# Optimization experiments

Measured on AMD Instinct MI355X. Metric: run time of the kernel, lower is better.

Reference implementation:

```python
import jax, jax.numpy as jnp
import numpy as np

L, B, S, D, H, FF = 6, 4, 1024, 256, 8, 128
DH = D // H
EPS = 1e-5


def _ln(x, w, b):
    m = x.mean(-1, keepdims=True)
    v = ((x - m) ** 2).mean(-1, keepdims=True)
    return (x - m) / jnp.sqrt(v + EPS) * w + b


def setup_inputs() -> dict:
    key = jax.random.key(0)
    ks = jax.random.split(key, 6)
    s = lambda k, shape: jax.random.normal(k, shape, jnp.float32) * 0.02
    return {
        "x": jax.random.normal(ks[0], (B, S, D), jnp.float32),
        "ln1_w": jnp.ones((L, D), jnp.float32),
        "ln1_b": jnp.zeros((L, D), jnp.float32),
        "wqkv": s(ks[1], (L, D, 3 * D)),   # qkv_linear, bias=False
        "wout": s(ks[2], (L, D, D)),       # out_linear, bias=False
        "ln2_w": jnp.ones((L, D), jnp.float32),
        "ln2_b": jnp.zeros((L, D), jnp.float32),
        "w1": s(ks[3], (L, D, 2 * FF)),    # Linear(d_model, 2*ff)
        "b1": jnp.zeros((L, 2 * FF), jnp.float32),
        "w2": s(ks[4], (L, FF, D)),        # Linear(ff, d_model)
        "b2": jnp.zeros((L, D), jnp.float32),
    }


def reference(x, ln1_w, ln1_b, wqkv, wout, ln2_w, ln2_b, w1, b1, w2, b2):
    attn_weights_list = []
    scale = 1.0 / jnp.sqrt(jnp.float32(DH))
    for i in range(L):
        # --- pre-norm multi-head attention ---
        xn = _ln(x, ln1_w[i], ln1_b[i])
        qkv = xn @ wqkv[i]                       # [B,S,3D]
        q, k, v = jnp.split(qkv, 3, axis=-1)
        rs = lambda t: t.reshape(B, S, H, DH).transpose(0, 2, 1, 3)  # b h s d
        q, k, v = rs(q), rs(k), rs(v)
        logits = jnp.einsum('bhid,bhjd->bhij', q, k) * scale
        aw = jax.nn.softmax(logits, axis=-1)     # [B,H,S,S] (dropout=0, eval)
        attn_weights_list.append(aw)
        o = jnp.einsum('bhij,bhjd->bhid', aw, v)
        o = o.transpose(0, 2, 1, 3).reshape(B, S, D) @ wout[i]
        x = x + o
        # --- pre-norm GEGLU FFN ---
        h = _ln(x, ln2_w[i], ln2_b[i]) @ w1[i] + b1[i]   # [B,S,2*FF]
        a, g = jnp.split(h, 2, axis=-1)
        x = x + (a * jax.nn.gelu(g, approximate=False)) @ w2[i] + b2[i]
    return x, jnp.stack(attn_weights_list)      # [B,S,D], [L,B,H,S,S]
```

## Files before the change

kernel.cpp:

```cpp
#include <hip/hip_runtime.h>
#include <hip/hip_bf16.h>

typedef __bf16 bf16x8 __attribute__((ext_vector_type(8)));
typedef __bf16 bf16x4 __attribute__((ext_vector_type(4)));
typedef __bf16 bf16x2 __attribute__((ext_vector_type(2)));
typedef float  f32x4  __attribute__((ext_vector_type(4)));

#define LAYERS 6
#define BATCH  4
#define SEQ    1024
#define DMODEL 256
#define NHEAD  8
#define DHEAD  32
#define FFDIM  128
#define ROWS   (BATCH*SEQ)
#define QKVN   (3*DMODEL)
#define QSCALE 0.2550348616f

static __device__ __forceinline__ bf16x8 ldg8(const __bf16* p) {
  return *reinterpret_cast<const bf16x8*>(p);
}
#define MFMA16(a, b, c) __builtin_amdgcn_mfma_f32_16x16x32_bf16((a), (b), (c), 0, 0, 0)

__global__ void k_prep(const float* __restrict__ wqkv, const float* __restrict__ wout,
                       const float* __restrict__ w1, const float* __restrict__ w2,
                       __bf16* __restrict__ wqkvT, __bf16* __restrict__ woutT,
                       __bf16* __restrict__ w1T, __bf16* __restrict__ w2T) {
  const int N1 = LAYERS * DMODEL * QKVN;
  const int N2 = LAYERS * DMODEL * DMODEL;
  const int N3 = LAYERS * DMODEL * 2 * FFDIM;
  const int N4 = LAYERS * FFDIM * DMODEL;
  int total = N1 + N2 + N3 + N4;
  for (int i = blockIdx.x * blockDim.x + threadIdx.x; i < total; i += gridDim.x * blockDim.x) {
    int j = i;
    if (j < N1) {
      int l = j / (DMODEL * QKVN), rc = j - l * (DMODEL * QKVN);
      int r = rc / QKVN, c = rc - r * QKVN;
      wqkvT[(size_t)l * DMODEL * QKVN + (size_t)c * DMODEL + r] = (__bf16)wqkv[j]; continue;
    } j -= N1;
    if (j < N2) {
      int l = j / (DMODEL * DMODEL), rc = j - l * (DMODEL * DMODEL);
      int r = rc / DMODEL, c = rc - r * DMODEL;
      woutT[(size_t)l * DMODEL * DMODEL + (size_t)c * DMODEL + r] = (__bf16)wout[j]; continue;
    } j -= N2;
    if (j < N3) {
      int l = j / (DMODEL * 2 * FFDIM), rc = j - l * (DMODEL * 2 * FFDIM);
      int r = rc / (2 * FFDIM), c = rc - r * (2 * FFDIM);
      w1T[(size_t)l * DMODEL * 2 * FFDIM + (size_t)c * DMODEL + r] = (__bf16)w1[j]; continue;
    } j -= N3;
    {
      int l = j / (FFDIM * DMODEL), rc = j - l * (FFDIM * DMODEL);
      int r = rc / DMODEL, c = rc - r * DMODEL;
      w2T[(size_t)l * FFDIM * DMODEL + (size_t)c * FFDIM + r] = (__bf16)w2[j];
    }
  }
}

__global__ __launch_bounds__(64) void k_ln(const float* __restrict__ x,
                                           const float* __restrict__ w,
                                           const float* __restrict__ b,
                                           __bf16* __restrict__ out) {
  int row = blockIdx.x, l = threadIdx.x;
  const float* xr = x + (size_t)row * DMODEL;
  float v[4];
  #pragma unroll
  for (int j = 0; j < 4; ++j) v[j] = xr[l + 64 * j];
  float s = v[0] + v[1] + v[2] + v[3];
  #pragma unroll
  for (int off = 32; off >= 1; off >>= 1) s += __shfl_xor(s, off);
  float mean = s * (1.0f / DMODEL);
  float sq = 0.f;
  #pragma unroll
  for (int j = 0; j < 4; ++j) { v[j] -= mean; sq += v[j] * v[j]; }
  #pragma unroll
  for (int off = 32; off >= 1; off >>= 1) sq += __shfl_xor(sq, off);
  float rstd = rsqrtf(sq * (1.0f / DMODEL) + 1e-5f);
  __bf16* orow = out + (size_t)row * DMODEL;
  #pragma unroll
  for (int j = 0; j < 4; ++j) {
    int c = l + 64 * j;
    orow[c] = (__bf16)(v[j] * rstd * w[c] + b[c]);
  }
}

__global__ __launch_bounds__(256) void k_qkv(const __bf16* __restrict__ xn,
                                             const __bf16* __restrict__ Bt,
                                             __bf16* __restrict__ qb,
                                             __bf16* __restrict__ kt,
                                             __bf16* __restrict__ vt) {
  int w = threadIdx.x >> 6, l = threadIdx.x & 63, lr = l & 15, lg = l >> 4;
  int m0 = blockIdx.x * 64 + w * 16;
  int n0 = blockIdx.y * 64;
  f32x4 acc[4] = {};
  const __bf16* ap = xn + (size_t)(m0 + lr) * DMODEL + 8 * lg;
  const __bf16* bp = Bt + (size_t)(n0 + lr) * DMODEL + 8 * lg;
  for (int kc = 0; kc < DMODEL; kc += 32) {
    bf16x8 a = ldg8(ap + kc);
    #pragma unroll
    for (int t = 0; t < 4; ++t) {
      bf16x8 b = ldg8(bp + (size_t)t * 16 * DMODEL + kc);
      acc[t] = MFMA16(a, b, acc[t]);
    }
  }
  int row = m0 + lg * 4;
  if (n0 < DMODEL) {
    #pragma unroll
    for (int t = 0; t < 4; ++t) {
      int col = n0 + t * 16 + lr;
      #pragma unroll
      for (int r = 0; r < 4; ++r)
        qb[(size_t)(row + r) * DMODEL + col] = (__bf16)(acc[t][r] * QSCALE);
    }
  } else if (n0 < 2 * DMODEL) {
    int b_ = row >> 10, s = row & (SEQ - 1);
    #pragma unroll
    for (int t = 0; t < 4; ++t) {
      int hdh = n0 - DMODEL + t * 16 + lr;
      int h = hdh >> 5, dh = hdh & 31;
      size_t base = ((size_t)(b_ * NHEAD + h) * SEQ + s) * DHEAD + dh;
      #pragma unroll
      for (int r = 0; r < 4; ++r) kt[base + (size_t)r * DHEAD] = (__bf16)acc[t][r];
    }
  } else {
    int b_ = row >> 10, s = row & (SEQ - 1);
    #pragma unroll
    for (int t = 0; t < 4; ++t) {
      int hdh = n0 - 2 * DMODEL + t * 16 + lr;
      int h = hdh >> 5, dh = hdh & 31;
      bf16x4 v4;
      #pragma unroll
      for (int r = 0; r < 4; ++r) v4[r] = (__bf16)acc[t][r];
      *reinterpret_cast<bf16x4*>(vt + ((size_t)(b_ * NHEAD + h) * DHEAD + dh) * SEQ + s) = v4;
    }
  }
}

__global__ __launch_bounds__(512, 4) void k_attn(const __bf16* __restrict__ qb,
                                                 const __bf16* __restrict__ kt,
                                                 const __bf16* __restrict__ vt,
                                                 __bf16* __restrict__ ob,
                                                 float* __restrict__ aw) {
  __shared__ __bf16 P[8][2][16][40];
  __shared__ float  Ssum[8][16];
  __shared__ float  OS[8][16][34];
  int bid = blockIdx.x;
  int swz = (bid & 7) * 256 + (bid >> 3);
  int qblk = swz & 63, h = (swz >> 6) & 7, b = swz >> 9;
  int w = threadIdx.x >> 6, l = threadIdx.x & 63, lr = l & 15, lg = l >> 4;
  int q0 = qblk * 16;
  bf16x8 qf = ldg8(qb + ((size_t)(b * SEQ) + q0 + lr) * DMODEL + h * DHEAD + 8 * lg);
  const __bf16* ktb = kt + (size_t)(b * NHEAD + h) * SEQ * DHEAD + 8 * lg;
  const __bf16* vtb = vt + (size_t)(b * NHEAD + h) * DHEAD * SEQ;
  f32x4 z = {};
  int kbeg = w * 128;

  f32x4 p[8];
  f32x4 accO[2] = {};

  #pragma unroll
  for (int j = 0; j < 4; ++j) {
    int kc = kbeg + j * 32;
    #pragma unroll
    for (int half = 0; half < 2; ++half) {
      int t = j * 2 + half;
      bf16x8 kf = ldg8(ktb + (size_t)(kc + half * 16 + lr) * DHEAD);
      f32x4 d = MFMA16(qf, kf, z);
      #pragma unroll
      for (int r = 0; r < 4; ++r) {
        p[t][r] = exp2f(d[r]);
        P[w][j & 1][lg * 4 + r][half * 16 + lr] = (__bf16)p[t][r];
      }
    }
    if (j > 0) {
      bf16x8 pf  = *reinterpret_cast<const bf16x8*>(&P[w][(j & 1) ^ 1][lr][8 * lg]);
      bf16x8 vf0 = ldg8(vtb + (size_t)lr * SEQ + (kc - 32) + 8 * lg);
      bf16x8 vf1 = ldg8(vtb + (size_t)(16 + lr) * SEQ + (kc - 32) + 8 * lg);
      accO[0] = MFMA16(pf, vf0, accO[0]);
      accO[1] = MFMA16(pf, vf1, accO[1]);
    }
  }
  {
    bf16x8 pf  = *reinterpret_cast<const bf16x8*>(&P[w][1][lr][8 * lg]);
    bf16x8 vf0 = ldg8(vtb + (size_t)lr * SEQ + (kbeg + 96) + 8 * lg);
    bf16x8 vf1 = ldg8(vtb + (size_t)(16 + lr) * SEQ + (kbeg + 96) + 8 * lg);
    accO[0] = MFMA16(pf, vf0, accO[0]);
    accO[1] = MFMA16(pf, vf1, accO[1]);
  }

  float s4[4] = {0.f, 0.f, 0.f, 0.f};
  #pragma unroll
  for (int t = 0; t < 8; ++t)
    #pragma unroll
    for (int r = 0; r < 4; ++r) s4[r] += p[t][r];
  #pragma unroll
  for (int off = 1; off < 16; off <<= 1) {
    #pragma unroll
    for (int r = 0; r < 4; ++r) s4[r] += __shfl_xor(s4[r], off);
  }
  if (lr == 0) {
    #pragma unroll
    for (int r = 0; r < 4; ++r) Ssum[w][lg * 4 + r] = s4[r];
  }
  __syncthreads();
  float rinv[4];
  #pragma unroll
  for (int r = 0; r < 4; ++r) {
    int row = lg * 4 + r;
    float s = Ssum[0][row] + Ssum[1][row] + Ssum[2][row] + Ssum[3][row]
            + Ssum[4][row] + Ssum[5][row] + Ssum[6][row] + Ssum[7][row];
    rinv[r] = 1.0f / s;
  }

  float* awb = aw + ((size_t)(b * NHEAD + h) * SEQ) * SEQ;
  #pragma unroll
  for (int t = 0; t < 8; ++t) {
    int k0 = kbeg + t * 16;
    #pragma unroll
    for (int r = 0; r < 4; ++r)
      __builtin_nontemporal_store(p[t][r] * rinv[r],
                                  &awb[(size_t)(q0 + lg * 4 + r) * SEQ + k0 + lr]);
  }

  #pragma unroll
  for (int t = 0; t < 2; ++t)
    #pragma unroll
    for (int r = 0; r < 4; ++r) OS[w][lg * 4 + r][t * 16 + lr] = accO[t][r] * rinv[r];
  __syncthreads();
  int row = threadIdx.x >> 5, col = threadIdx.x & 31;
  float o = 0.f;
  #pragma unroll
  for (int ww = 0; ww < 8; ++ww) o += OS[ww][row][col];
  ob[((size_t)(b * SEQ) + q0 + row) * DMODEL + h * DHEAD + col] = (__bf16)o;
}

template <int LAST>
__global__ __launch_bounds__(512) void k_pf(const __bf16* __restrict__ ob,
                                            const __bf16* __restrict__ woutT,
                                            const float* __restrict__ xres,
                                            const float* __restrict__ ln2w,
                                            const float* __restrict__ ln2b,
                                            const __bf16* __restrict__ w1t,
                                            const float* __restrict__ b1,
                                            const __bf16* __restrict__ w2t,
                                            const float* __restrict__ b2,
                                            float* __restrict__ x32out,
                                            const float* __restrict__ lnw_n,
                                            const float* __restrict__ lnb_n,
                                            const __bf16* __restrict__ wqkvT_n,
                                            __bf16* __restrict__ qb,
                                            __bf16* __restrict__ kt,
                                            __bf16* __restrict__ vt,
                                            float* __restrict__ xout) {
  __shared__ float  xs[16][268];
  __shared__ __bf16 XN[16][264];
  __shared__ __bf16 G[16][136];
  __shared__ __bf16 HT[16][136];
  int w = threadIdx.x >> 6, l = threadIdx.x & 63, lr = l & 15, lg = l >> 4;
  int m0 = blockIdx.x * 16;
  {
    int n0 = w * 32;
    f32x4 acc[2] = {};
    const __bf16* ap = ob + (size_t)(m0 + lr) * DMODEL + 8 * lg;
    const __bf16* bp = woutT + (size_t)(n0 + lr) * DMODEL + 8 * lg;
    for (int kc = 0; kc < DMODEL; kc += 32) {
      bf16x8 a = ldg8(ap + kc);
      #pragma unroll
      for (int t = 0; t < 2; ++t)
        acc[t] = MFMA16(a, ldg8(bp + (size_t)t * 16 * DMODEL + kc), acc[t]);
    }
    #pragma unroll
    for (int t = 0; t < 2; ++t) {
      int col = n0 + t * 16 + lr;
      #pragma unroll
      for (int r = 0; r < 4; ++r) {
        int row = lg * 4 + r;
        xs[row][col] = acc[t][r] + xres[(size_t)(m0 + row) * DMODEL + col];
      }
    }
  }
  __syncthreads();
  #pragma unroll
  for (int rr = 0; rr < 2; ++rr) {
    int row = w * 2 + rr;
    f32x4 v = *reinterpret_cast<const f32x4*>(&xs[row][4 * l]);
    float s = v[0] + v[1] + v[2] + v[3];
    #pragma unroll
    for (int off = 32; off >= 1; off >>= 1) s += __shfl_xor(s, off);
    float mean = s * (1.0f / DMODEL);
    float sq = 0.f;
    f32x4 c;
    #pragma unroll
    for (int j = 0; j < 4; ++j) { c[j] = v[j] - mean; sq += c[j] * c[j]; }
    #pragma unroll
    for (int off = 32; off >= 1; off >>= 1) sq += __shfl_xor(sq, off);
    float rstd = rsqrtf(sq * (1.0f / DMODEL) + 1e-5f);
    f32x4 lwv = *reinterpret_cast<const f32x4*>(&ln2w[4 * l]);
    f32x4 lbv = *reinterpret_cast<const f32x4*>(&ln2b[4 * l]);
    bf16x4 o4;
    #pragma unroll
    for (int j = 0; j < 4; ++j) o4[j] = (__bf16)(c[j] * rstd * lwv[j] + lbv[j]);
    *reinterpret_cast<bf16x4*>(&XN[row][4 * l]) = o4;
  }
  __syncthreads();
  int n0f = w * 32;
  f32x4 acc1[2] = {};
  {
    const __bf16* bp = w1t + (size_t)(n0f + lr) * DMODEL + 8 * lg;
    for (int kc = 0; kc < DMODEL; kc += 32) {
      bf16x8 a = *reinterpret_cast<const bf16x8*>(&XN[lr][kc + 8 * lg]);
      #pragma unroll
      for (int t = 0; t < 2; ++t)
        acc1[t] = MFMA16(a, ldg8(bp + (size_t)t * 16 * DMODEL + kc), acc1[t]);
    }
  }
  if (w >= 4) {
    #pragma unroll
    for (int t = 0; t < 2; ++t) {
      int col = n0f + t * 16 + lr;
      #pragma unroll
      for (int r = 0; r < 4; ++r) {
        float g = acc1[t][r] + b1[col];
        float ge = 0.5f * g * (1.0f + erff(g * 0.70710678118654752f));
        G[lg * 4 + r][col - 128] = (__bf16)ge;
      }
    }
  }
  __syncthreads();
  if (w < 4) {
    #pragma unroll
    for (int t = 0; t < 2; ++t) {
      int col = n0f + t * 16 + lr;
      #pragma unroll
      for (int r = 0; r < 4; ++r) {
        float a1 = acc1[t][r] + b1[col];
        HT[lg * 4 + r][col] = (__bf16)(a1 * (float)G[lg * 4 + r][col]);
      }
    }
  }
  __syncthreads();
  {
    f32x4 acc2[2] = {};
    const __bf16* bp = w2t + (size_t)(n0f + lr) * FFDIM + 8 * lg;
    for (int kc = 0; kc < FFDIM; kc += 32) {
      bf16x8 a2 = *reinterpret_cast<const bf16x8*>(&HT[lr][kc + 8 * lg]);
      #pragma unroll
      for (int t = 0; t < 2; ++t)
        acc2[t] = MFMA16(a2, ldg8(bp + (size_t)t * 16 * FFDIM + kc), acc2[t]);
    }
    #pragma unroll
    for (int t = 0; t < 2; ++t) {
      int col = n0f + t * 16 + lr;
      #pragma unroll
      for (int r = 0; r < 4; ++r) {
        int row = lg * 4 + r;
        xs[row][col] = acc2[t][r] + b2[col] + xs[row][col];
      }
    }
  }
  __syncthreads();
  #pragma unroll
  for (int rr = 0; rr < 2; ++rr) {
    int row = w * 2 + rr;
    f32x4 v = *reinterpret_cast<const f32x4*>(&xs[row][4 * l]);
    if (LAST) {
      *reinterpret_cast<f32x4*>(&xout[(size_t)(m0 + row) * DMODEL + 4 * l]) = v;
    } else {
      float s = v[0] + v[1] + v[2] + v[3];
      #pragma unroll
      for (int off = 32; off >= 1; off >>= 1) s += __shfl_xor(s, off);
      float mean = s * (1.0f / DMODEL);
      float sq = 0.f;
      f32x4 c;
      #pragma unroll
      for (int j = 0; j < 4; ++j) { c[j] = v[j] - mean; sq += c[j] * c[j]; }
      #pragma unroll
      for (int off = 32; off >= 1; off >>= 1) sq += __shfl_xor(sq, off);
      float rstd = rsqrtf(sq * (1.0f / DMODEL) + 1e-5f);
      *reinterpret_cast<f32x4*>(&x32out[(size_t)(m0 + row) * DMODEL + 4 * l]) = v;
      f32x4 lwv = *reinterpret_cast<const f32x4*>(&lnw_n[4 * l]);
      f32x4 lbv = *reinterpret_cast<const f32x4*>(&lnb_n[4 * l]);
      bf16x4 o4;
      #pragma unroll
      for (int j = 0; j < 4; ++j) o4[j] = (__bf16)(c[j] * rstd * lwv[j] + lbv[j]);
      *reinterpret_cast<bf16x4*>(&XN[row][4 * l]) = o4;
    }
  }
  if (!LAST) {
    __syncthreads();
    f32x4 acc[6] = {};
    {
      const __bf16* bp = wqkvT_n + (size_t)(w * 96 + lr) * DMODEL + 8 * lg;
      for (int kc = 0; kc < DMODEL; kc += 32) {
        bf16x8 a = *reinterpret_cast<const bf16x8*>(&XN[lr][kc + 8 * lg]);
        #pragma unroll
        for (int t = 0; t < 6; ++t)
          acc[t] = MFMA16(a, ldg8(bp + (size_t)t * 16 * DMODEL + kc), acc[t]);
      }
    }
    int row = m0 + lg * 4;
    int b_ = row >> 10, s = row & (SEQ - 1);
    #pragma unroll
    for (int t = 0; t < 6; ++t) {
      int col = w * 96 + t * 16 + lr;
      if (col < DMODEL) {
        #pragma unroll
        for (int r = 0; r < 4; ++r)
          qb[(size_t)(row + r) * DMODEL + col] = (__bf16)(acc[t][r] * QSCALE);
      } else if (col < 2 * DMODEL) {
        int hdh = col - DMODEL;
        int h = hdh >> 5, dh = hdh & 31;
        size_t base = ((size_t)(b_ * NHEAD + h) * SEQ + s) * DHEAD + dh;
        #pragma unroll
        for (int r = 0; r < 4; ++r) kt[base + (size_t)r * DHEAD] = (__bf16)acc[t][r];
      } else {
        int hdh = col - 2 * DMODEL;
        int h = hdh >> 5, dh = hdh & 31;
        bf16x4 v4;
        #pragma unroll
        for (int r = 0; r < 4; ++r) v4[r] = (__bf16)acc[t][r];
        *reinterpret_cast<bf16x4*>(vt + ((size_t)(b_ * NHEAD + h) * DHEAD + dh) * SEQ + s) = v4;
      }
    }
  }
}

static inline size_t align256(size_t x) { return (x + 255) & ~(size_t)255; }

extern "C" void kernel_launch(void* const* d_in, const int* in_sizes, int n_in,
                              void* d_out, int out_size, void* d_ws, size_t ws_size,
                              hipStream_t stream) {
  const float* x_in = (const float*)d_in[0];
  const float* ln1w = (const float*)d_in[1];
  const float* ln1b = (const float*)d_in[2];
  const float* wqkv = (const float*)d_in[3];
  const float* wout = (const float*)d_in[4];
  const float* ln2w = (const float*)d_in[5];
  const float* ln2b = (const float*)d_in[6];
  const float* w1   = (const float*)d_in[7];
  const float* b1   = (const float*)d_in[8];
  const float* w2   = (const float*)d_in[9];
  const float* b2   = (const float*)d_in[10];
  float* out = (float*)d_out;

  char* p = (char*)d_ws;
  float*  x32   = (float*)p;  p += align256((size_t)ROWS * DMODEL * 4);
  __bf16* xn    = (__bf16*)p; p += align256((size_t)ROWS * DMODEL * 2);
  __bf16* qb    = (__bf16*)p; p += align256((size_t)ROWS * DMODEL * 2);
  __bf16* kt    = (__bf16*)p; p += align256((size_t)ROWS * DMODEL * 2);
  __bf16* vt    = (__bf16*)p; p += align256((size_t)ROWS * DMODEL * 2);
  __bf16* ob    = (__bf16*)p; p += align256((size_t)ROWS * DMODEL * 2);
  __bf16* wqkvT = (__bf16*)p; p += align256((size_t)LAYERS * DMODEL * QKVN * 2);
  __bf16* woutT = (__bf16*)p; p += align256((size_t)LAYERS * DMODEL * DMODEL * 2);
  __bf16* w1T   = (__bf16*)p; p += align256((size_t)LAYERS * DMODEL * 2 * FFDIM * 2);
  __bf16* w2T   = (__bf16*)p; p += align256((size_t)LAYERS * FFDIM * DMODEL * 2);

  k_prep<<<2048, 256, 0, stream>>>(wqkv, wout, w1, w2, wqkvT, woutT, w1T, w2T);
  k_ln<<<ROWS, 64, 0, stream>>>(x_in, ln1w, ln1b, xn);
  k_qkv<<<dim3(ROWS / 64, QKVN / 64), 256, 0, stream>>>(xn, wqkvT, qb, kt, vt);

  const size_t AW_LAYER = (size_t)BATCH * NHEAD * SEQ * SEQ;
  for (int i = 0; i < LAYERS; ++i) {
    float* aw_l = out + (size_t)ROWS * DMODEL + (size_t)i * AW_LAYER;
    k_attn<<<SEQ / 16 * NHEAD * BATCH, 512, 0, stream>>>(qb, kt, vt, ob, aw_l);
    const float* xres = (i == 0) ? x_in : x32;
    if (i < LAYERS - 1) {
      k_pf<0><<<ROWS / 16, 512, 0, stream>>>(
          ob, woutT + (size_t)i * DMODEL * DMODEL, xres,
          ln2w + i * DMODEL, ln2b + i * DMODEL,
          w1T + (size_t)i * DMODEL * 2 * FFDIM, b1 + i * 2 * FFDIM,
          w2T + (size_t)i * FFDIM * DMODEL, b2 + i * DMODEL,
          x32, ln1w + (i + 1) * DMODEL, ln1b + (i + 1) * DMODEL,
          wqkvT + (size_t)(i + 1) * DMODEL * QKVN, qb, kt, vt, nullptr);
    } else {
      k_pf<1><<<ROWS / 16, 512, 0, stream>>>(
          ob, woutT + (size_t)i * DMODEL * DMODEL, xres,
          ln2w + i * DMODEL, ln2b + i * DMODEL,
          w1T + (size_t)i * DMODEL * 2 * FFDIM, b1 + i * 2 * FFDIM,
          w2T + (size_t)i * FFDIM * DMODEL, b2 + i * DMODEL,
          x32, nullptr, nullptr, nullptr, nullptr, nullptr, nullptr, out);
    }
  }
}
```

Before: 463.0 us.

## Recompute QK logits in two passes to free registers and raise attention occupancy

```diff
diff --git a/kernel.cpp b/kernel.cpp
--- a/kernel.cpp
+++ b/kernel.cpp
@@ -135,7 +135,7 @@
   }
 }
 
-__global__ __launch_bounds__(512, 4) void k_attn(const __bf16* __restrict__ qb,
+__global__ __launch_bounds__(512, 6) void k_attn(const __bf16* __restrict__ qb,
                                                  const __bf16* __restrict__ kt,
                                                  const __bf16* __restrict__ vt,
                                                  __bf16* __restrict__ ob,
@@ -154,30 +154,63 @@
   f32x4 z = {};
   int kbeg = w * 128;
 
-  f32x4 p[8];
+  float s4[4] = {0.f, 0.f, 0.f, 0.f};
+  #pragma unroll 4
+  for (int t = 0; t < 8; ++t) {
+    bf16x8 kf = ldg8(ktb + (size_t)(kbeg + t * 16 + lr) * DHEAD);
+    f32x4 d = MFMA16(qf, kf, z);
+    #pragma unroll
+    for (int r = 0; r < 4; ++r) s4[r] += exp2f(d[r]);
+  }
+  #pragma unroll
+  for (int off = 1; off < 16; off <<= 1) {
+    #pragma unroll
+    for (int r = 0; r < 4; ++r) s4[r] += __shfl_xor(s4[r], off);
+  }
+  if (lr == 0) {
+    #pragma unroll
+    for (int r = 0; r < 4; ++r) Ssum[w][lg * 4 + r] = s4[r];
+  }
+  __syncthreads();
+  float rinv[4];
+  #pragma unroll
+  for (int r = 0; r < 4; ++r) {
+    int row = lg * 4 + r;
+    float s = Ssum[0][row] + Ssum[1][row] + Ssum[2][row] + Ssum[3][row]
+            + Ssum[4][row] + Ssum[5][row] + Ssum[6][row] + Ssum[7][row];
+    rinv[r] = 1.0f / s;
+  }
+
+  float* awb = aw + ((size_t)(b * NHEAD + h) * SEQ) * SEQ;
+
+#define QK_TILE(KC, BUF)                                                          \
+  {                                                                               \
+    _Pragma("unroll")                                                             \
+    for (int half = 0; half < 2; ++half) {                                        \
+      int k0 = (KC) + half * 16;                                                  \
+      bf16x8 kf = ldg8(ktb + (size_t)(k0 + lr) * DHEAD);                          \
+      f32x4 d = MFMA16(qf, kf, z);                                                \
+      _Pragma("unroll")                                                           \
+      for (int r = 0; r < 4; ++r) {                                               \
+        float pv = exp2f(d[r]);                                                   \
+        __builtin_nontemporal_store(pv * rinv[r],                                 \
+            &awb[(size_t)(q0 + lg * 4 + r) * SEQ + k0 + lr]);                     \
+        P[w][BUF][lg * 4 + r][half * 16 + lr] = (__bf16)pv;                       \
+      }                                                                           \
+    }                                                                             \
+  }
+
   f32x4 accO[2] = {};
-
-  #pragma unroll
-  for (int j = 0; j < 4; ++j) {
+  QK_TILE(kbeg, 0)
+  #pragma unroll
+  for (int j = 1; j < 4; ++j) {
     int kc = kbeg + j * 32;
-    #pragma unroll
-    for (int half = 0; half < 2; ++half) {
-      int t = j * 2 + half;
-      bf16x8 kf = ldg8(ktb + (size_t)(kc + half * 16 + lr) * DHEAD);
-      f32x4 d = MFMA16(qf, kf, z);
-      #pragma unroll
-      for (int r = 0; r < 4; ++r) {
-        p[t][r] = exp2f(d[r]);
-        P[w][j & 1][lg * 4 + r][half * 16 + lr] = (__bf16)p[t][r];
-      }
-    }
-    if (j > 0) {
-      bf16x8 pf  = *reinterpret_cast<const bf16x8*>(&P[w][(j & 1) ^ 1][lr][8 * lg]);
-      bf16x8 vf0 = ldg8(vtb + (size_t)lr * SEQ + (kc - 32) + 8 * lg);
-      bf16x8 vf1 = ldg8(vtb + (size_t)(16 + lr) * SEQ + (kc - 32) + 8 * lg);
-      accO[0] = MFMA16(pf, vf0, accO[0]);
-      accO[1] = MFMA16(pf, vf1, accO[1]);
-    }
+    bf16x8 pf  = *reinterpret_cast<const bf16x8*>(&P[w][(j - 1) & 1][lr][8 * lg]);
+    bf16x8 vf0 = ldg8(vtb + (size_t)lr * SEQ + (kc - 32) + 8 * lg);
+    bf16x8 vf1 = ldg8(vtb + (size_t)(16 + lr) * SEQ + (kc - 32) + 8 * lg);
+    QK_TILE(kc, j & 1)
+    accO[0] = MFMA16(pf, vf0, accO[0]);
+    accO[1] = MFMA16(pf, vf1, accO[1]);
   }
   {
     bf16x8 pf  = *reinterpret_cast<const bf16x8*>(&P[w][1][lr][8 * lg]);
@@ -186,40 +219,7 @@
     accO[0] = MFMA16(pf, vf0, accO[0]);
     accO[1] = MFMA16(pf, vf1, accO[1]);
   }
-
-  float s4[4] = {0.f, 0.f, 0.f, 0.f};
-  #pragma unroll
-  for (int t = 0; t < 8; ++t)
-    #pragma unroll
-    for (int r = 0; r < 4; ++r) s4[r] += p[t][r];
-  #pragma unroll
-  for (int off = 1; off < 16; off <<= 1) {
-    #pragma unroll
-    for (int r = 0; r < 4; ++r) s4[r] += __shfl_xor(s4[r], off);
-  }
-  if (lr == 0) {
-    #pragma unroll
-    for (int r = 0; r < 4; ++r) Ssum[w][lg * 4 + r] = s4[r];
-  }
-  __syncthreads();
-  float rinv[4];
-  #pragma unroll
-  for (int r = 0; r < 4; ++r) {
-    int row = lg * 4 + r;
-    float s = Ssum[0][row] + Ssum[1][row] + Ssum[2][row] + Ssum[3][row]
-            + Ssum[4][row] + Ssum[5][row] + Ssum[6][row] + Ssum[7][row];
-    rinv[r] = 1.0f / s;
-  }
-
-  float* awb = aw + ((size_t)(b * NHEAD + h) * SEQ) * SEQ;
-  #pragma unroll
-  for (int t = 0; t < 8; ++t) {
-    int k0 = kbeg + t * 16;
-    #pragma unroll
-    for (int r = 0; r < 4; ++r)
-      __builtin_nontemporal_store(p[t][r] * rinv[r],
-                                  &awb[(size_t)(q0 + lg * 4 + r) * SEQ + k0 + lr]);
-  }
+#undef QK_TILE
 
   #pragma unroll
   for (int t = 0; t < 2; ++t)
```

After: 458.3 us. No clear change (-1.0%).
